# Performance work log

Measured on AMD Instinct MI355X. Metric: run time of the kernel, lower is better.

Reference implementation:

```python
import jax, jax.numpy as jnp
import numpy as np

D = 512      # input_size == per-head embed_size (wide attention)
H = 8        # num_attn_heads


def setup_inputs() -> dict:
    key = jax.random.key(0)
    ks = jax.random.split(key, 8)
    B, S = 2, 2048
    scale = 1.0 / np.sqrt(D)
    return {
        "Xin_q": jax.random.normal(ks[0], (B, S, D), dtype=jnp.float32),
        "Xin_k": jax.random.normal(ks[1], (B, S, D), dtype=jnp.float32),
        "Xin_v": jax.random.normal(ks[2], (B, S, D), dtype=jnp.float32),
        # per-head projection weights, stored as [H, D_in, D_out] (bias-free)
        "Wq": jax.random.normal(ks[3], (H, D, D), dtype=jnp.float32) * scale,
        "Wk": jax.random.normal(ks[4], (H, D, D), dtype=jnp.float32) * scale,
        "Wv": jax.random.normal(ks[5], (H, D, D), dtype=jnp.float32) * scale,
        # output projection: concat(H*D) -> D, with bias
        "Wz": jax.random.normal(ks[6], (H * D, D), dtype=jnp.float32) * (1.0 / np.sqrt(H * D)),
        "bz": jax.random.normal(ks[7], (D,), dtype=jnp.float32) * 0.01,
    }


def reference(Xin_q, Xin_k, Xin_v, Wq, Wk, Wv, Wz, bz):
    B, Sq, _ = Xin_q.shape
    inv4 = 1.0 / (D ** 0.25)  # each of Q and K scaled by embed_size**(1/4)
    # project all heads at once: [B,H,S,D]
    q = jnp.einsum("bsd,hde->bhse", Xin_q, Wq) * inv4
    k = jnp.einsum("bsd,hde->bhse", Xin_k, Wk) * inv4
    v = jnp.einsum("bsd,hde->bhse", Xin_v, Wv)
    attn = jax.nn.softmax(jnp.einsum("bhqe,bhke->bhqk", q, k), axis=-1)
    z = jnp.einsum("bhqk,bhke->bhqe", attn, v)        # [B,H,S,D]
    # concat heads along last dim (head-major order matches torch.cat over the head loop)
    z = jnp.transpose(z, (0, 2, 1, 3)).reshape(B, Sq, H * D)
    out = z @ Wz + bz                                  # [B,S,D]
    attn_avg = jnp.mean(attn, axis=1)                  # [B,Sq,Skv]
    return out, attn_avg
```

## Files before the change

### kernel.cpp

```cpp
#include <hip/hip_runtime.h>
#include <math.h>

#define BB 2
#define SS 2048
#define D_ 512
#define H_ 8
#define MS (BB * SS)
#define HD (H_ * D_)

typedef short bf16x8 __attribute__((ext_vector_type(8)));
typedef float f32x4 __attribute__((ext_vector_type(4)));

__device__ inline unsigned short f2bf(float f) {
    union { float f; unsigned u; } x{f};
    unsigned r = x.u + 0x7fff + ((x.u >> 16) & 1);
    return (unsigned short)(r >> 16);
}
__device__ inline float bf2f(unsigned short u) {
    union { unsigned u; float f; } x{(unsigned)u << 16};
    return x.f;
}

constexpr size_t SZ_X   = (size_t)MS * D_ * 2;
constexpr size_t SZ_W   = (size_t)H_ * D_ * D_ * 2;
constexpr size_t SZ_WZ  = (size_t)HD * D_ * 2;
constexpr size_t SZ_QK  = (size_t)H_ * MS * D_ * 2;
constexpr size_t SZ_SC  = (size_t)H_ * BB * SS * SS * 2;
constexpr size_t SZ_Z   = (size_t)MS * HD * 2;
constexpr size_t SZ_OP  = (size_t)2 * MS * D_ * 4;
constexpr size_t OFF_XQ  = 0;
constexpr size_t OFF_XK  = OFF_XQ + SZ_X;
constexpr size_t OFF_XV  = OFF_XK + SZ_X;
constexpr size_t OFF_WQT = OFF_XV + SZ_X;
constexpr size_t OFF_WKT = OFF_WQT + SZ_W;
constexpr size_t OFF_WVT = OFF_WKT + SZ_W;
constexpr size_t OFF_WZT = OFF_WVT + SZ_W;
constexpr size_t OFF_QB  = OFF_WZT + SZ_WZ;
constexpr size_t OFF_KB  = OFF_QB + SZ_QK;
constexpr size_t OFF_VT  = OFF_KB + SZ_QK;
constexpr size_t OFF_SC  = OFF_VT + SZ_QK;
constexpr size_t OFF_Z   = OFF_SC + SZ_SC;
constexpr size_t OFF_OP  = OFF_Z + SZ_Z;
constexpr size_t WS_TOTAL = OFF_OP + SZ_OP;
__device__ __align__(256) unsigned char g_ws[WS_TOTAL];

__device__ inline void gl2lds16(const unsigned short* g, unsigned short* l) {
    __builtin_amdgcn_global_load_lds(
        (const __attribute__((address_space(1))) void*)g,
        (__attribute__((address_space(3))) void*)l, 16, 0, 0);
}

__global__ __launch_bounds__(256) void gemm_bt_k(
    const unsigned short* __restrict__ A, const unsigned short* __restrict__ B,
    void* __restrict__ Cv, int K, int ldA, int ldB, int ldC,
    long sA1, long sA2, long sB1, long sB2, long sC1, long sC2, int d2,
    float alpha, const float* __restrict__ bias, int outBf16)
{
    __shared__ unsigned short As[128 * 64];
    __shared__ unsigned short Bs[128 * 64];
    const int gx = gridDim.x, gy = gridDim.y, gz = gridDim.z;
    int bx, by, bz;
    if (((gy * gz) & 7) == 0) {
        const long L = blockIdx.x + (long)gx * (blockIdx.y + (long)gy * blockIdx.z);
        const int d = (int)(L & 7);
        const long s = L >> 3;
        bx = (int)(s % gx);
        const long yz = d + 8 * (s / gx);
        by = (int)(yz % gy);
        bz = (int)(yz / gy);
    } else {
        bx = blockIdx.x; by = blockIdx.y; bz = blockIdx.z;
    }
    const int z1 = bz / d2, z2 = bz % d2;
    A += z1 * sA1 + z2 * sA2;
    B += z1 * sB1 + z2 * sB2;
    const long cOff = z1 * sC1 + z2 * sC2;
    const int m0 = by * 128, n0 = bx * 128;
    const int tid = threadIdx.x;
    const int w = tid >> 6, l = tid & 63;

    const int sr = l >> 3;
    const int sq = (l & 7) ^ sr;
    const unsigned short* ga = A + (long)(m0 + w * 32 + sr) * ldA + sq * 8;
    const unsigned short* gb = B + (long)(n0 + w * 32 + sr) * ldB + sq * 8;
    unsigned short* laA = As + w * 2048;
    unsigned short* laB = Bs + w * 2048;

    const int wm = w >> 1, wn = w & 1;
    const int q = l >> 4;
    const int sl = l & 7;
    const int mA = wm * 64 + (l & 15);
    const int nB = wn * 64 + (l & 15);
    const int s0 = ((q) ^ sl) * 8;
    const int s1 = ((q + 4) ^ sl) * 8;
    const unsigned short* pa0 = As + mA * 64 + s0;
    const unsigned short* pa1 = As + mA * 64 + s1;
    const unsigned short* pb0 = Bs + nB * 64 + s0;
    const unsigned short* pb1 = Bs + nB * 64 + s1;

    f32x4 acc[4][4] = {};
    for (int kk = 0; kk < K; kk += 64) {
#pragma unroll
        for (int i = 0; i < 4; i++) {
            gl2lds16(ga + (long)i * 8 * ldA, laA + i * 512);
            gl2lds16(gb + (long)i * 8 * ldB, laB + i * 512);
        }
        ga += 64; gb += 64;
        __syncthreads();
        bf16x8 af[4], bf[4];
#pragma unroll
        for (int i = 0; i < 4; i++) {
            af[i] = *(const bf16x8*)(pa0 + i * 1024);
            bf[i] = *(const bf16x8*)(pb0 + i * 1024);
        }
#pragma unroll
        for (int mi = 0; mi < 4; mi++)
#pragma unroll
            for (int ni = 0; ni < 4; ni++)
                acc[mi][ni] = __builtin_amdgcn_mfma_f32_16x16x32_bf16(
                    af[mi], bf[ni], acc[mi][ni], 0, 0, 0);
#pragma unroll
        for (int i = 0; i < 4; i++) {
            af[i] = *(const bf16x8*)(pa1 + i * 1024);
            bf[i] = *(const bf16x8*)(pb1 + i * 1024);
        }
#pragma unroll
        for (int mi = 0; mi < 4; mi++)
#pragma unroll
            for (int ni = 0; ni < 4; ni++)
                acc[mi][ni] = __builtin_amdgcn_mfma_f32_16x16x32_bf16(
                    af[mi], bf[ni], acc[mi][ni], 0, 0, 0);
        __syncthreads();
    }

    const int rowB = m0 + wm * 64 + q * 4;
    const int colB = n0 + wn * 64 + (l & 15);
    if (outBf16) {
        unsigned short* C = (unsigned short*)Cv + cOff;
#pragma unroll
        for (int mi = 0; mi < 4; mi++)
#pragma unroll
            for (int ni = 0; ni < 4; ni++) {
                const int col = colB + ni * 16;
#pragma unroll
                for (int rg = 0; rg < 4; rg++)
                    C[(long)(rowB + mi * 16 + rg) * ldC + col] =
                        f2bf(alpha * acc[mi][ni][rg]);
            }
    } else {
        float* C = (float*)Cv + cOff;
#pragma unroll
        for (int ni = 0; ni < 4; ni++) {
            const int col = colB + ni * 16;
            const float bs = bias ? bias[col] : 0.f;
#pragma unroll
            for (int mi = 0; mi < 4; mi++)
#pragma unroll
                for (int rg = 0; rg < 4; rg++)
                    C[(long)(rowB + mi * 16 + rg) * ldC + col] =
                        alpha * acc[mi][ni][rg] + bs;
        }
    }
}

__global__ __launch_bounds__(256) void cvt3_k(
    const float* __restrict__ i0, const float* __restrict__ i1, const float* __restrict__ i2,
    unsigned short* __restrict__ o0, unsigned short* __restrict__ o1,
    unsigned short* __restrict__ o2, long n4)
{
    const float* in = blockIdx.z == 0 ? i0 : (blockIdx.z == 1 ? i1 : i2);
    unsigned short* out = blockIdx.z == 0 ? o0 : (blockIdx.z == 1 ? o1 : o2);
    long i = (long)blockIdx.x * 256 + threadIdx.x;
    if (i >= n4) return;
    float4 v = ((const float4*)in)[i];
    ushort4 o;
    o.x = f2bf(v.x); o.y = f2bf(v.y); o.z = f2bf(v.z); o.w = f2bf(v.w);
    ((ushort4*)out)[i] = o;
}

__global__ __launch_bounds__(256) void transcvt3_k(
    const float* __restrict__ i0, const float* __restrict__ i1, const float* __restrict__ i2,
    unsigned short* __restrict__ o0, unsigned short* __restrict__ o1,
    unsigned short* __restrict__ o2)
{
    __shared__ float t[32][33];
    const int zt = blockIdx.z >> 3, h = blockIdx.z & 7;
    const float* in = (zt == 0 ? i0 : (zt == 1 ? i1 : i2)) + (long)h * D_ * D_;
    unsigned short* out = (zt == 0 ? o0 : (zt == 1 ? o1 : o2)) + (long)h * D_ * D_;
    const int r0 = blockIdx.y * 32, c0 = blockIdx.x * 32;
    const int tr = threadIdx.x >> 5, tc = threadIdx.x & 31;
#pragma unroll
    for (int i = 0; i < 4; i++)
        t[tr + i * 8][tc] = in[(long)(r0 + tr + i * 8) * D_ + c0 + tc];
    __syncthreads();
#pragma unroll
    for (int i = 0; i < 4; i++)
        out[(long)(c0 + tr + i * 8) * D_ + r0 + tc] = f2bf(t[tc][tr + i * 8]);
}

__global__ __launch_bounds__(256) void transcvt_k(
    const float* __restrict__ in, unsigned short* __restrict__ out, int R, int C)
{
    __shared__ float t[32][33];
    const int r0 = blockIdx.y * 32, c0 = blockIdx.x * 32;
    const int tr = threadIdx.x >> 5, tc = threadIdx.x & 31;
#pragma unroll
    for (int i = 0; i < 4; i++)
        t[tr + i * 8][tc] = in[(long)(r0 + tr + i * 8) * C + c0 + tc];
    __syncthreads();
#pragma unroll
    for (int i = 0; i < 4; i++)
        out[(long)(c0 + tr + i * 8) * R + r0 + tc] = f2bf(t[tc][tr + i * 8]);
}

__device__ inline float wred_max(float v) {
#pragma unroll
    for (int o = 32; o; o >>= 1) v = fmaxf(v, __shfl_down(v, o));
    return v;
}
__device__ inline float wred_sum(float v) {
#pragma unroll
    for (int o = 32; o; o >>= 1) v += __shfl_down(v, o);
    return v;
}
__global__ __launch_bounds__(256) void softmax_avg_k(
    unsigned short* __restrict__ SP, float* __restrict__ avg)
{
    const int blk = blockIdx.x;
    const int b = blk >> 11, s = blk & (SS - 1);
    const int tid = threadIdx.x;
    __shared__ float red[4];
    float av[8] = {};
    const int t0 = tid * 8;
    for (int h = 0; h < H_; h++) {
        const long rowOff = ((long)(h * BB + b) * SS + s) * SS + t0;
        const ushort4 u0 = *(const ushort4*)(SP + rowOff);
        const ushort4 u1 = *(const ushort4*)(SP + rowOff + 4);
        float vals[8] = {bf2f(u0.x), bf2f(u0.y), bf2f(u0.z), bf2f(u0.w),
                         bf2f(u1.x), bf2f(u1.y), bf2f(u1.z), bf2f(u1.w)};
        float m = vals[0];
#pragma unroll
        for (int i = 1; i < 8; i++) m = fmaxf(m, vals[i]);
        float wm = wred_max(m);
        if ((tid & 63) == 0) red[tid >> 6] = wm;
        __syncthreads();
        m = fmaxf(fmaxf(red[0], red[1]), fmaxf(red[2], red[3]));
        __syncthreads();
        float sum = 0.f;
#pragma unroll
        for (int i = 0; i < 8; i++) { vals[i] = __expf(vals[i] - m); sum += vals[i]; }
        float wsum = wred_sum(sum);
        if ((tid & 63) == 0) red[tid >> 6] = wsum;
        __syncthreads();
        sum = red[0] + red[1] + red[2] + red[3];
        __syncthreads();
        const float inv = 1.0f / sum;
        ushort4 o0, o1;
        float p0 = vals[0] * inv, p1 = vals[1] * inv, p2 = vals[2] * inv, p3 = vals[3] * inv;
        float p4 = vals[4] * inv, p5 = vals[5] * inv, p6 = vals[6] * inv, p7 = vals[7] * inv;
        av[0] += p0; av[1] += p1; av[2] += p2; av[3] += p3;
        av[4] += p4; av[5] += p5; av[6] += p6; av[7] += p7;
        o0.x = f2bf(p0); o0.y = f2bf(p1); o0.z = f2bf(p2); o0.w = f2bf(p3);
        o1.x = f2bf(p4); o1.y = f2bf(p5); o1.z = f2bf(p6); o1.w = f2bf(p7);
        *(ushort4*)(SP + rowOff) = o0;
        *(ushort4*)(SP + rowOff + 4) = o1;
    }
    const long aOff = ((long)b * SS + s) * SS + t0;
    float4 a0 = {av[0] * 0.125f, av[1] * 0.125f, av[2] * 0.125f, av[3] * 0.125f};
    float4 a1 = {av[4] * 0.125f, av[5] * 0.125f, av[6] * 0.125f, av[7] * 0.125f};
    *(float4*)(avg + aOff) = a0;
    *(float4*)(avg + aOff + 4) = a1;
}

__global__ __launch_bounds__(256) void addbias_k(
    const float* __restrict__ p0, const float* __restrict__ p1,
    const float* __restrict__ bz, float* __restrict__ out)
{
    const long n4 = (long)MS * D_ / 4;
    long i = (long)blockIdx.x * 256 + threadIdx.x;
    if (i >= n4) return;
    const int col4 = (int)((i * 4) & (D_ - 1));
    float4 a = ((const float4*)p0)[i];
    float4 b = ((const float4*)p1)[i];
    float4 c = *(const float4*)(bz + col4);
    float4 o = {a.x + b.x + c.x, a.y + b.y + c.y, a.z + b.z + c.z, a.w + b.w + c.w};
    ((float4*)out)[i] = o;
}

extern "C" void kernel_launch(void* const* d_in, const int* in_sizes, int n_in,
                              void* d_out, int out_size, void* d_ws, size_t ws_size,
                              hipStream_t stream)
{
    const float* Xq = (const float*)d_in[0];
    const float* Xk = (const float*)d_in[1];
    const float* Xv = (const float*)d_in[2];
    const float* Wq = (const float*)d_in[3];
    const float* Wk = (const float*)d_in[4];
    const float* Wv = (const float*)d_in[5];
    const float* Wz = (const float*)d_in[6];
    const float* bz = (const float*)d_in[7];

    float* out      = (float*)d_out;
    float* attn_avg = out + (long)MS * D_;

    unsigned char* ws = nullptr;
    (void)hipGetSymbolAddress((void**)&ws, HIP_SYMBOL(g_ws));
    unsigned short* Xbq = (unsigned short*)(ws + OFF_XQ);
    unsigned short* Xbk = (unsigned short*)(ws + OFF_XK);
    unsigned short* Xbv = (unsigned short*)(ws + OFF_XV);
    unsigned short* Wqt = (unsigned short*)(ws + OFF_WQT);
    unsigned short* Wkt = (unsigned short*)(ws + OFF_WKT);
    unsigned short* Wvt = (unsigned short*)(ws + OFF_WVT);
    unsigned short* Wzt = (unsigned short*)(ws + OFF_WZT);
    unsigned short* qb  = (unsigned short*)(ws + OFF_QB);
    unsigned short* vT  = (unsigned short*)(ws + OFF_VT);
    unsigned short* scb = (unsigned short*)(ws + OFF_SC);
    unsigned short* zal = (unsigned short*)(ws + OFF_Z);
    float*          opp = (float*)(ws + OFF_OP);

    const float inv4 = 1.0f / powf((float)D_, 0.25f);

    const long n4x = (long)MS * D_ / 4;
    cvt3_k<<<dim3((n4x + 255) / 256, 1, 3), 256, 0, stream>>>(
        Xq, Xk, Xv, Xbq, Xbk, Xbv, n4x);
    transcvt3_k<<<dim3(16, 16, 24), 256, 0, stream>>>(Wq, Wk, Wv, Wqt, Wkt, Wvt);
    transcvt_k<<<dim3(16, 128, 1), 256, 0, stream>>>(Wz, Wzt, HD, D_);

    gemm_bt_k<<<dim3(4, 32, 16), 256, 0, stream>>>(
        Xbq, Wqt, qb, D_, D_, D_, D_,
        (long)MS * D_, 0, (long)H_ * D_ * D_, (long)D_ * D_,
        (long)H_ * MS * D_, (long)MS * D_, 8, inv4, nullptr, 1);
    gemm_bt_k<<<dim3(16, 4, 16), 256, 0, stream>>>(
        Wvt, Xbv, vT, D_, D_, D_, SS,
        (long)D_ * D_, 0, 0, (long)SS * D_, (long)2 * D_ * SS, (long)D_ * SS, 2,
        1.0f, nullptr, 1);

    gemm_bt_k<<<dim3(16, 16, 16), 256, 0, stream>>>(
        qb, qb + (long)H_ * MS * D_, scb, D_, D_, D_, SS,
        (long)MS * D_, (long)SS * D_, (long)MS * D_, (long)SS * D_,
        (long)2 * SS * SS, (long)SS * SS, 2, 1.0f, nullptr, 1);

    softmax_avg_k<<<dim3(BB * SS), 256, 0, stream>>>(scb, attn_avg);

    gemm_bt_k<<<dim3(4, 16, 16), 256, 0, stream>>>(
        scb, vT, zal, SS, SS, SS, HD,
        (long)2 * SS * SS, (long)SS * SS, (long)2 * D_ * SS, (long)D_ * SS,
        512, (long)SS * HD, 2, 1.0f, nullptr, 1);

    gemm_bt_k<<<dim3(4, 32, 2), 256, 0, stream>>>(
        zal, Wzt, opp, HD / 2, HD, HD, D_,
        0, 2048, 0, 2048, 0, (long)MS * D_, 2, 1.0f, nullptr, 0);
    const long n4o = (long)MS * D_ / 4;
    addbias_k<<<dim3((n4o + 255) / 256), 256, 0, stream>>>(
        opp, opp + (long)MS * D_, bz, out);
}
```

Before: 518.8 us.

## Fuse exp into score GEMM and defer softmax normalization to PV GEMM

The QK^T GEMM epilogue now applies exp directly to the scores. The softmax kernel becomes a read-only pass: it computes row sums, writes per-row inverse sums and accumulates the head-averaged attention. The PV GEMM scales each output row by the stored inverse sum, so the large probability matrix is no longer rewritten. This removes a full write of the bf16 score tensor and the max-reduction pass. In exchange it drops max subtraction, which risks exp overflow when scores are large, and stores unnormalized exponentials in bf16.

New measurement: 497.0 us. 1.04x faster.

```diff
diff --git a/kernel.cpp b/kernel.cpp
--- a/kernel.cpp
+++ b/kernel.cpp
@@ -28,6 +28,7 @@
 constexpr size_t SZ_SC  = (size_t)H_ * BB * SS * SS * 2;
 constexpr size_t SZ_Z   = (size_t)MS * HD * 2;
 constexpr size_t SZ_OP  = (size_t)2 * MS * D_ * 4;
+constexpr size_t SZ_LV  = (size_t)H_ * BB * SS * 4;
 constexpr size_t OFF_XQ  = 0;
 constexpr size_t OFF_XK  = OFF_XQ + SZ_X;
 constexpr size_t OFF_XV  = OFF_XK + SZ_X;
@@ -41,7 +42,8 @@
 constexpr size_t OFF_SC  = OFF_VT + SZ_QK;
 constexpr size_t OFF_Z   = OFF_SC + SZ_SC;
 constexpr size_t OFF_OP  = OFF_Z + SZ_Z;
-constexpr size_t WS_TOTAL = OFF_OP + SZ_OP;
+constexpr size_t OFF_LV  = OFF_OP + SZ_OP;
+constexpr size_t WS_TOTAL = OFF_LV + SZ_LV;
 __device__ __align__(256) unsigned char g_ws[WS_TOTAL];
 
 __device__ inline void gl2lds16(const unsigned short* g, unsigned short* l) {
@@ -54,7 +56,8 @@
     const unsigned short* __restrict__ A, const unsigned short* __restrict__ B,
     void* __restrict__ Cv, int K, int ldA, int ldB, int ldC,
     long sA1, long sA2, long sB1, long sB2, long sC1, long sC2, int d2,
-    float alpha, const float* __restrict__ bias, int outBf16)
+    float alpha, const float* __restrict__ bias, int outBf16, int doExp,
+    const float* __restrict__ rowScale, long sR1, long sR2)
 {
     __shared__ unsigned short As[128 * 64];
     __shared__ unsigned short Bs[128 * 64];
@@ -75,6 +78,7 @@
     A += z1 * sA1 + z2 * sA2;
     B += z1 * sB1 + z2 * sB2;
     const long cOff = z1 * sC1 + z2 * sC2;
+    const long rsOff = z1 * sR1 + z2 * sR2;
     const int m0 = by * 128, n0 = bx * 128;
     const int tid = threadIdx.x;
     const int w = tid >> 6, l = tid & 63;
@@ -138,15 +142,19 @@
     if (outBf16) {
         unsigned short* C = (unsigned short*)Cv + cOff;
 #pragma unroll
-        for (int mi = 0; mi < 4; mi++)
-#pragma unroll
-            for (int ni = 0; ni < 4; ni++) {
-                const int col = colB + ni * 16;
-#pragma unroll
-                for (int rg = 0; rg < 4; rg++)
-                    C[(long)(rowB + mi * 16 + rg) * ldC + col] =
-                        f2bf(alpha * acc[mi][ni][rg]);
+        for (int mi = 0; mi < 4; mi++) {
+#pragma unroll
+            for (int rg = 0; rg < 4; rg++) {
+                const int row = rowB + mi * 16 + rg;
+                const float rs = rowScale ? rowScale[rsOff + row] : 1.0f;
+#pragma unroll
+                for (int ni = 0; ni < 4; ni++) {
+                    float v = alpha * acc[mi][ni][rg];
+                    if (doExp) v = __expf(v);
+                    C[(long)row * ldC + colB + ni * 16] = f2bf(v * rs);
+                }
             }
+        }
     } else {
         float* C = (float*)Cv + cOff;
 #pragma unroll
@@ -213,18 +221,14 @@
         out[(long)(c0 + tr + i * 8) * R + r0 + tc] = f2bf(t[tc][tr + i * 8]);
 }
 
-__device__ inline float wred_max(float v) {
-#pragma unroll
-    for (int o = 32; o; o >>= 1) v = fmaxf(v, __shfl_down(v, o));
-    return v;
-}
 __device__ inline float wred_sum(float v) {
 #pragma unroll
     for (int o = 32; o; o >>= 1) v += __shfl_down(v, o);
     return v;
 }
-__global__ __launch_bounds__(256) void softmax_avg_k(
-    unsigned short* __restrict__ SP, float* __restrict__ avg)
+__global__ __launch_bounds__(256) void sumavg_k(
+    const unsigned short* __restrict__ E, float* __restrict__ avg,
+    float* __restrict__ linv)
 {
     const int blk = blockIdx.x;
     const int b = blk >> 11, s = blk & (SS - 1);
@@ -234,40 +238,27 @@
     const int t0 = tid * 8;
     for (int h = 0; h < H_; h++) {
         const long rowOff = ((long)(h * BB + b) * SS + s) * SS + t0;
-        const ushort4 u0 = *(const ushort4*)(SP + rowOff);
-        const ushort4 u1 = *(const ushort4*)(SP + rowOff + 4);
+        const ushort4 u0 = *(const ushort4*)(E + rowOff);
+        const ushort4 u1 = *(const ushort4*)(E + rowOff + 4);
         float vals[8] = {bf2f(u0.x), bf2f(u0.y), bf2f(u0.z), bf2f(u0.w),
                          bf2f(u1.x), bf2f(u1.y), bf2f(u1.z), bf2f(u1.w)};
-        float m = vals[0];
-#pragma unroll
-        for (int i = 1; i < 8; i++) m = fmaxf(m, vals[i]);
-        float wm = wred_max(m);
-        if ((tid & 63) == 0) red[tid >> 6] = wm;
-        __syncthreads();
-        m = fmaxf(fmaxf(red[0], red[1]), fmaxf(red[2], red[3]));
-        __syncthreads();
         float sum = 0.f;
 #pragma unroll
-        for (int i = 0; i < 8; i++) { vals[i] = __expf(vals[i] - m); sum += vals[i]; }
+        for (int i = 0; i < 8; i++) sum += vals[i];
         float wsum = wred_sum(sum);
         if ((tid & 63) == 0) red[tid >> 6] = wsum;
         __syncthreads();
         sum = red[0] + red[1] + red[2] + red[3];
         __syncthreads();
         const float inv = 1.0f / sum;
-        ushort4 o0, o1;
-        float p0 = vals[0] * inv, p1 = vals[1] * inv, p2 = vals[2] * inv, p3 = vals[3] * inv;
-        float p4 = vals[4] * inv, p5 = vals[5] * inv, p6 = vals[6] * inv, p7 = vals[7] * inv;
-        av[0] += p0; av[1] += p1; av[2] += p2; av[3] += p3;
-        av[4] += p4; av[5] += p5; av[6] += p6; av[7] += p7;
-        o0.x = f2bf(p0); o0.y = f2bf(p1); o0.z = f2bf(p2); o0.w = f2bf(p3);
-        o1.x = f2bf(p4); o1.y = f2bf(p5); o1.z = f2bf(p6); o1.w = f2bf(p7);
-        *(ushort4*)(SP + rowOff) = o0;
-        *(ushort4*)(SP + rowOff + 4) = o1;
+        if (tid == 0) linv[(long)(h * BB + b) * SS + s] = inv;
+        const float invH = inv * 0.125f;
+#pragma unroll
+        for (int i = 0; i < 8; i++) av[i] += vals[i] * invH;
     }
     const long aOff = ((long)b * SS + s) * SS + t0;
-    float4 a0 = {av[0] * 0.125f, av[1] * 0.125f, av[2] * 0.125f, av[3] * 0.125f};
-    float4 a1 = {av[4] * 0.125f, av[5] * 0.125f, av[6] * 0.125f, av[7] * 0.125f};
+    float4 a0 = {av[0], av[1], av[2], av[3]};
+    float4 a1 = {av[4], av[5], av[6], av[7]};
     *(float4*)(avg + aOff) = a0;
     *(float4*)(avg + aOff + 4) = a1;
 }
@@ -317,6 +308,7 @@
     unsigned short* scb = (unsigned short*)(ws + OFF_SC);
     unsigned short* zal = (unsigned short*)(ws + OFF_Z);
     float*          opp = (float*)(ws + OFF_OP);
+    float*          linv = (float*)(ws + OFF_LV);
 
     const float inv4 = 1.0f / powf((float)D_, 0.25f);
 
@@ -329,27 +321,28 @@
     gemm_bt_k<<<dim3(4, 32, 16), 256, 0, stream>>>(
         Xbq, Wqt, qb, D_, D_, D_, D_,
         (long)MS * D_, 0, (long)H_ * D_ * D_, (long)D_ * D_,
-        (long)H_ * MS * D_, (long)MS * D_, 8, inv4, nullptr, 1);
+        (long)H_ * MS * D_, (long)MS * D_, 8, inv4, nullptr, 1, 0, nullptr, 0, 0);
     gemm_bt_k<<<dim3(16, 4, 16), 256, 0, stream>>>(
         Wvt, Xbv, vT, D_, D_, D_, SS,
         (long)D_ * D_, 0, 0, (long)SS * D_, (long)2 * D_ * SS, (long)D_ * SS, 2,
-        1.0f, nullptr, 1);
+        1.0f, nullptr, 1, 0, nullptr, 0, 0);
 
     gemm_bt_k<<<dim3(16, 16, 16), 256, 0, stream>>>(
         qb, qb + (long)H_ * MS * D_, scb, D_, D_, D_, SS,
         (long)MS * D_, (long)SS * D_, (long)MS * D_, (long)SS * D_,
-        (long)2 * SS * SS, (long)SS * SS, 2, 1.0f, nullptr, 1);
-
-    softmax_avg_k<<<dim3(BB * SS), 256, 0, stream>>>(scb, attn_avg);
+        (long)2 * SS * SS, (long)SS * SS, 2, 1.0f, nullptr, 1, 1, nullptr, 0, 0);
+
+    sumavg_k<<<dim3(BB * SS), 256, 0, stream>>>(scb, attn_avg, linv);
 
     gemm_bt_k<<<dim3(4, 16, 16), 256, 0, stream>>>(
         scb, vT, zal, SS, SS, SS, HD,
         (long)2 * SS * SS, (long)SS * SS, (long)2 * D_ * SS, (long)D_ * SS,
-        512, (long)SS * HD, 2, 1.0f, nullptr, 1);
+        512, (long)SS * HD, 2, 1.0f, nullptr, 1, 0,
+        linv, (long)BB * SS, (long)SS);
 
     gemm_bt_k<<<dim3(4, 32, 2), 256, 0, stream>>>(
         zal, Wzt, opp, HD / 2, HD, HD, D_,
-        0, 2048, 0, 2048, 0, (long)MS * D_, 2, 1.0f, nullptr, 0);
+        0, 2048, 0, 2048, 0, (long)MS * D_, 2, 1.0f, nullptr, 0, 0, nullptr, 0, 0);
     const long n4o = (long)MS * D_ / 4;
     addbias_k<<<dim3((n4o + 255) / 256), 256, 0, stream>>>(
         opp, opp + (long)MS * D_, bz, out);
```
